# Performance work log

Measured on AMD Instinct MI355X. Metric: run time of the kernel, lower is better.

## Reference

```python
import jax, jax.numpy as jnp
import numpy as np

B, C, H, W = 16, 256, 64, 64
NH = 4                      # num_heads
HD = C // NH                # head_dim = 64
G = 32                      # GroupNorm groups
EPS = 1e-5


def setup_inputs() -> dict:
    key = jax.random.key(0)
    ks = jax.random.split(key, 7)
    x = jax.random.normal(ks[0], (B, C, H, W), dtype=jnp.float32)
    gn_w = jnp.ones((C,), dtype=jnp.float32)
    gn_b = jnp.zeros((C,), dtype=jnp.float32)
    qkv_w = jax.random.normal(ks[1], (3 * C, C), dtype=jnp.float32) * 0.02
    qkv_b = jnp.zeros((3 * C,), dtype=jnp.float32)
    out_w = jax.random.normal(ks[2], (C, C), dtype=jnp.float32) * 0.02
    out_b = jnp.zeros((C,), dtype=jnp.float32)
    return {"x": x, "gn_w": gn_w, "gn_b": gn_b, "qkv_w": qkv_w,
            "qkv_b": qkv_b, "out_w": out_w, "out_b": out_b}


def _group_norm(x, w, b):
    # x: (B, C, H, W); normalize over each of G groups of channels (+ spatial)
    Bx, Cx, Hx, Wx = x.shape
    xr = x.reshape(Bx, G, -1)
    mean = xr.mean(axis=-1, keepdims=True)
    var = xr.var(axis=-1, keepdims=True)
    h = ((xr - mean) * jax.lax.rsqrt(var + EPS)).reshape(Bx, Cx, Hx, Wx)
    return h * w[None, :, None, None] + b[None, :, None, None]


def reference(x, gn_w, gn_b, qkv_w, qkv_b, out_w, out_b):
    Bx, Cx, Hx, Wx = x.shape
    N = Hx * Wx
    h = _group_norm(x, gn_w, gn_b)
    # 1x1 conv == channel matmul
    qkv = jnp.einsum('oc,bchw->bohw', qkv_w, h) + qkv_b[None, :, None, None]
    q, k, v = jnp.split(qkv, 3, axis=1)
    # b (h d) y x -> b h d n
    q = q.reshape(Bx, NH, HD, N)
    k = k.reshape(Bx, NH, HD, N)
    v = v.reshape(Bx, NH, HD, N)
    q = jax.nn.softmax(q, axis=-1)   # over spatial positions n
    k = jax.nn.softmax(k, axis=-2)   # over head_dim d
    # context = k @ v^T : (b,h,d,d)
    context = jnp.einsum('bhdn,bhen->bhde', k, v)
    # out = context^T @ q : (b,h,d,n)
    out = jnp.einsum('bhde,bhdn->bhen', context, q)
    out = out.reshape(Bx, Cx, Hx, Wx)
    out = jnp.einsum('oc,bchw->bohw', out_w, out) + out_b[None, :, None, None]
    return x + out
```

## Files before the change

### kernel.cpp

```cpp
#include <hip/hip_runtime.h>


typedef __bf16 bf16x8 __attribute__((ext_vector_type(8)));
typedef __bf16 bf16x4 __attribute__((ext_vector_type(4)));
typedef __bf16 bf16x2 __attribute__((ext_vector_type(2)));
typedef float  f32x4  __attribute__((ext_vector_type(4)));

__device__ __forceinline__ float wave_red_sum(float v) {
#pragma unroll
    for (int off = 32; off > 0; off >>= 1) v += __shfl_xor(v, off, 64);
    return v;
}
__device__ __forceinline__ float wave_red_max(float v) {
#pragma unroll
    for (int off = 32; off > 0; off >>= 1) v = fmaxf(v, __shfl_xor(v, off, 64));
    return v;
}

__global__ __launch_bounds__(256)
void gn_stats_kernel(const float* __restrict__ x, const float* __restrict__ gw,
                     const float* __restrict__ gb, const float* __restrict__ qw,
                     float2* __restrict__ scsh, __bf16* __restrict__ wb)
{
    const int blk = blockIdx.x;
    const int b = blk >> 5, g = blk & 31;
    const int tid = threadIdx.x;
    const int lane = tid & 63, wid = tid >> 6;
    const size_t xbase = ((size_t)(b * 256 + g * 8)) * 4096;

    {
        const int ci = (blk * 256 + tid) * 2;
        if (ci < 196608) {
            const float2 f = *(const float2*)(qw + ci);
            bf16x2 t; t[0] = (__bf16)f.x; t[1] = (__bf16)f.y;
            *(bf16x2*)(wb + ci) = t;
        }
    }

    float s1 = 0.f, s2 = 0.f;
#pragma unroll
    for (int it = 0; it < 32; it++) {
        const int idx = (it * 256 + tid) * 4;
        const float4 v4 = *(const float4*)(x + xbase + idx);
        s1 += v4.x + v4.y + v4.z + v4.w;
        s2 += v4.x * v4.x + v4.y * v4.y + v4.z * v4.z + v4.w * v4.w;
    }
    __shared__ float red[8];
    float s1w = wave_red_sum(s1);
    float s2w = wave_red_sum(s2);
    if (lane == 0) { red[wid] = s1w; red[4 + wid] = s2w; }
    __syncthreads();
    const float mean = (red[0] + red[1] + red[2] + red[3]) * (1.0f / 32768.0f);
    const float ms   = (red[4] + red[5] + red[6] + red[7]) * (1.0f / 32768.0f);
    const float inv  = rsqrtf(fmaxf(ms - mean * mean, 0.f) + 1e-5f);

    if (tid < 8) {
        const int c = g * 8 + tid;
        const float sc = gw[c] * inv;
        const float sh = gb[c] - mean * sc;
        scsh[b * 256 + c] = make_float2(sc, sh);
    }
}

__global__ __launch_bounds__(256)
void gemm1_kernel(const __bf16* __restrict__ wbf,
                  const float* __restrict__ x,
                  const float* __restrict__ bias,
                  const float2* __restrict__ scsh,
                  __bf16* __restrict__ qkv)
{
    __shared__ __align__(16) __bf16 lds_bt[64 * 264];
    __shared__ __align__(16) char  lds_a[256 * 64];
    __shared__ float2 lscsh[256];

    const int tid  = threadIdx.x;
    const int lane = tid & 63;
    const int wid  = tid >> 6;
    const int quad = lane >> 4;
    const int tcol = lane & 15;
    const int wm   = wid * 64;
    const int n0   = blockIdx.x * 64;
    const int b    = n0 >> 12;
    const int nn   = n0 & 4095;

    lscsh[tid] = scsh[b * 256 + tid];
    __syncthreads();

    const int sn = tid & 63;
    const int cq = tid >> 6;
    const float* xs = x + (size_t)b * 1048576 + nn + sn;
#pragma unroll
    for (int iter = 0; iter < 4; iter++) {
        const int cbase = cq * 64 + iter * 16;
        bf16x8 o0, o1;
#pragma unroll
        for (int j = 0; j < 16; j++) {
            const int c = cbase + j;
            const float2 ss = lscsh[c];
            const float f = xs[(size_t)c * 4096];
            const __bf16 v = (__bf16)(f * ss.x + ss.y);
            if (j < 8) o0[j] = v; else o1[j - 8] = v;
        }
        __bf16* dst = &lds_bt[sn * 264 + cbase];
        *(bf16x8*)dst       = o0;
        *(bf16x8*)(dst + 8) = o1;
    }

    const int r_   = tid >> 1;
    const int ah   = tid & 1;
    const int h16  = ah * 16;
    const int aswz = (r_ >> 1) & 3;
    const int ch0  = (((ah * 2)     + aswz) & 3) * 16;
    const int ch1  = (((ah * 2 + 1) + aswz) & 3) * 16;
    const __bf16* abase = wbf + (size_t)r_ * 256 + h16;

    bf16x8 a0 = *(const bf16x8*)(abase);
    bf16x8 a1 = *(const bf16x8*)(abase + 8);
    bf16x8 a2 = *(const bf16x8*)(abase + 32768);
    bf16x8 a3 = *(const bf16x8*)(abase + 32768 + 8);

    for (int mt = 0; mt < 3; mt++) {
        f32x4 acc[4][4];
#pragma unroll
        for (int i = 0; i < 4; i++)
#pragma unroll
            for (int j = 0; j < 4; j++) acc[i][j] = {0.f, 0.f, 0.f, 0.f};

        for (int kt = 0; kt < 256; kt += 32) {
            __syncthreads();
            *(bf16x8*)&lds_a[r_ * 64         + ch0] = a0;
            *(bf16x8*)&lds_a[r_ * 64         + ch1] = a1;
            *(bf16x8*)&lds_a[(r_ + 128) * 64 + ch0] = a2;
            *(bf16x8*)&lds_a[(r_ + 128) * 64 + ch1] = a3;
            __syncthreads();

            const int last = (kt == 224);
            const int nkt  = last ? 0 : kt + 32;
            const int nmt  = last ? mt + 1 : mt;
            if (nmt < 3) {
                const __bf16* ap = abase + (size_t)nmt * 65536 + nkt;
                a0 = *(const bf16x8*)(ap);
                a1 = *(const bf16x8*)(ap + 8);
                a2 = *(const bf16x8*)(ap + 32768);
                a3 = *(const bf16x8*)(ap + 32768 + 8);
            }

            bf16x8 af[4];
#pragma unroll
            for (int mi = 0; mi < 4; mi++) {
                const int m = wm + mi * 16 + tcol;
                af[mi] = *(const bf16x8*)&lds_a[m * 64
                         + ((quad + ((m >> 1) & 3)) & 3) * 16];
            }
            bf16x8 bfr[4];
#pragma unroll
            for (int ni = 0; ni < 4; ni++)
                bfr[ni] = *(const bf16x8*)&lds_bt[(ni * 16 + tcol) * 264
                                                 + kt + quad * 8];
#pragma unroll
            for (int mi = 0; mi < 4; mi++)
#pragma unroll
                for (int ni = 0; ni < 4; ni++)
                    acc[mi][ni] = __builtin_amdgcn_mfma_f32_16x16x32_bf16(
                        af[mi], bfr[ni], acc[mi][ni], 0, 0, 0);
        }

#pragma unroll
        for (int mi = 0; mi < 4; mi++) {
#pragma unroll
            for (int r = 0; r < 4; r++) {
                const int grow = mt * 256 + wm + mi * 16 + quad * 4 + r;
                const float bv = bias[grow];
#pragma unroll
                for (int ni = 0; ni < 4; ni++) {
                    const int gcol = n0 + ni * 16 + tcol;
                    qkv[(size_t)grow * 65536 + gcol] = (__bf16)(acc[mi][ni][r] + bv);
                }
            }
        }
    }
}

__global__ __launch_bounds__(256)
void qstats_kernel(const __bf16* __restrict__ qkv, float2* __restrict__ qst)
{
    const int o = blockIdx.x >> 4;
    const int b = blockIdx.x & 15;
    const int tid = threadIdx.x;
    const int lane = tid & 63, wid = tid >> 6;
    const size_t base = (size_t)o * 65536 + (size_t)b * 4096;

    float v[16];
    float m = -INFINITY;
#pragma unroll
    for (int s = 0; s < 16; s++) {
        v[s] = (float)qkv[base + s * 256 + tid];
        m = fmaxf(m, v[s]);
    }
    __shared__ float red[4];
    float wmx = wave_red_max(m);
    if (lane == 0) red[wid] = wmx;
    __syncthreads();
    m = fmaxf(fmaxf(red[0], red[1]), fmaxf(red[2], red[3]));
    __syncthreads();
    float sum = 0.f;
#pragma unroll
    for (int s = 0; s < 16; s++) sum += __expf(v[s] - m);
    float wsm = wave_red_sum(sum);
    if (lane == 0) red[wid] = wsm;
    __syncthreads();
    if (tid == 0)
        qst[o * 16 + b] = make_float2(m, 1.0f / (red[0] + red[1] + red[2] + red[3]));
}

__global__ __launch_bounds__(256)
void ctx_mfma_kernel(const __bf16* __restrict__ qkv, float* __restrict__ ctx)
{
    const int bh = blockIdx.x >> 3, kc = blockIdx.x & 7;
    const int b = bh >> 2, hh = bh & 3;
    __shared__ __align__(16) __bf16 lk[64 * 72], lv[64 * 72];
    __shared__ float smax[4][64], ssum[4][64];
    const int tid = threadIdx.x;
    const int lane = tid & 63, wid = tid >> 6;
    const int quad = lane >> 4, tcol = lane & 15;
    const int eh = (wid & 1) * 32, dh = (wid >> 1) * 32;
    const int col = tid & 63, dq = tid >> 6;
    const int sd = tid >> 2, snn = (tid & 3) * 16;

    f32x4 acc[2][2];
#pragma unroll
    for (int i = 0; i < 2; i++)
#pragma unroll
        for (int j = 0; j < 2; j++) acc[i][j] = {0.f, 0.f, 0.f, 0.f};

    const size_t kbase = (size_t)(256 + hh * 64) * 65536 + (size_t)b * 4096 + kc * 512;
    const size_t vbase = (size_t)(512 + hh * 64) * 65536 + (size_t)b * 4096 + kc * 512;

    for (int nc = 0; nc < 512; nc += 64) {
        __syncthreads();
        {
            const __bf16* ks = qkv + kbase + (size_t)sd * 65536 + nc + snn;
            *(bf16x8*)&lk[sd * 72 + snn]     = *(const bf16x8*)ks;
            *(bf16x8*)&lk[sd * 72 + snn + 8] = *(const bf16x8*)(ks + 8);
            const __bf16* vs = qkv + vbase + (size_t)sd * 65536 + nc + snn;
            *(bf16x8*)&lv[sd * 72 + snn]     = *(const bf16x8*)vs;
            *(bf16x8*)&lv[sd * 72 + snn + 8] = *(const bf16x8*)(vs + 8);
        }
        __syncthreads();

        float kvv[16];
        float pm = -INFINITY;
#pragma unroll
        for (int i = 0; i < 16; i++) {
            kvv[i] = (float)lk[(dq * 16 + i) * 72 + col];
            pm = fmaxf(pm, kvv[i]);
        }
        smax[dq][col] = pm;
        __syncthreads();
        const float m = fmaxf(fmaxf(smax[0][col], smax[1][col]),
                              fmaxf(smax[2][col], smax[3][col]));
        float ps = 0.f;
#pragma unroll
        for (int i = 0; i < 16; i++) { kvv[i] = __expf(kvv[i] - m); ps += kvv[i]; }
        ssum[dq][col] = ps;
        __syncthreads();
        const float inv = 1.0f / (ssum[0][col] + ssum[1][col] + ssum[2][col] + ssum[3][col]);
#pragma unroll
        for (int i = 0; i < 16; i++)
            lk[(dq * 16 + i) * 72 + col] = (__bf16)(kvv[i] * inv);
        __syncthreads();

#pragma unroll
        for (int k2 = 0; k2 < 64; k2 += 32) {
            bf16x8 af[2], bfr[2];
#pragma unroll
            for (int mi = 0; mi < 2; mi++)
                af[mi] = *(const bf16x8*)&lv[(eh + mi * 16 + tcol) * 72 + k2 + quad * 8];
#pragma unroll
            for (int ni = 0; ni < 2; ni++)
                bfr[ni] = *(const bf16x8*)&lk[(dh + ni * 16 + tcol) * 72 + k2 + quad * 8];
#pragma unroll
            for (int mi = 0; mi < 2; mi++)
#pragma unroll
                for (int ni = 0; ni < 2; ni++)
                    acc[mi][ni] = __builtin_amdgcn_mfma_f32_16x16x32_bf16(
                        af[mi], bfr[ni], acc[mi][ni], 0, 0, 0);
        }
    }
    float* cb = ctx + (size_t)bh * 4096;
#pragma unroll
    for (int mi = 0; mi < 2; mi++)
#pragma unroll
        for (int ni = 0; ni < 2; ni++)
#pragma unroll
            for (int r = 0; r < 4; r++) {
                const int e = eh + mi * 16 + quad * 4 + r;
                const int d = dh + ni * 16 + tcol;
                atomicAdd(&cb[e * 64 + d], acc[mi][ni][r]);
            }
}

__global__ __launch_bounds__(256)
void w2_kernel(const float* __restrict__ ctx, const float* __restrict__ out_w,
               __bf16* __restrict__ w2)
{
    const int bh = blockIdx.x;
    const int b = bh >> 2, hh = bh & 3;
    const int tid = threadIdx.x;

    __shared__ __align__(16) float lctx[4096];
    const float* csrc = ctx + (size_t)bh * 4096;
#pragma unroll
    for (int i = 0; i < 4; i++)
        ((float4*)lctx)[tid + i * 256] = ((const float4*)csrc)[tid + i * 256];
    __syncthreads();

    float acc[64];
#pragma unroll
    for (int d = 0; d < 64; d++) acc[d] = 0.f;

    const float* wrow = out_w + (size_t)tid * 256 + hh * 64;
    for (int e = 0; e < 64; e++) {
        const float w = wrow[e];
#pragma unroll
        for (int d4 = 0; d4 < 64; d4 += 4) {
            const float4 c4 = *(const float4*)&lctx[e * 64 + d4];
            acc[d4 + 0] += w * c4.x;
            acc[d4 + 1] += w * c4.y;
            acc[d4 + 2] += w * c4.z;
            acc[d4 + 3] += w * c4.w;
        }
    }
    __bf16* dst = w2 + (size_t)b * 65536 + (size_t)tid * 256 + hh * 64;
#pragma unroll
    for (int d4 = 0; d4 < 64; d4 += 4) {
        bf16x4 t;
        t[0] = (__bf16)acc[d4 + 0]; t[1] = (__bf16)acc[d4 + 1];
        t[2] = (__bf16)acc[d4 + 2]; t[3] = (__bf16)acc[d4 + 3];
        *(bf16x4*)(dst + d4) = t;
    }
}

__global__ __launch_bounds__(256)
void gemm2_kernel(const __bf16* __restrict__ w2,
                  const __bf16* __restrict__ qkv,
                  const float2* __restrict__ qst,
                  const float* __restrict__ bias,
                  const float* __restrict__ xres,
                  float* __restrict__ out)
{
    __shared__ __align__(16) __bf16 lds_bt[128 * 264];
    __shared__ __align__(16) __bf16 lds_a[128 * 40];
    __shared__ float2 lqst[256];

    const int tid  = threadIdx.x;
    const int lane = tid & 63;
    const int wid  = tid >> 6;
    const int quad = lane >> 4;
    const int tcol = lane & 15;
    const int wm   = (wid & 1) * 64;
    const int wn   = (wid >> 1) * 64;
    const int n0   = blockIdx.x * 128;
    const int b    = n0 >> 12;

    lqst[tid] = qst[tid * 16 + b];
    __syncthreads();

    const int sn    = tid & 127;
    const int chalf = tid >> 7;
    const int swz   = (sn >> 3) & 3;
#pragma unroll
    for (int iter = 0; iter < 8; iter++) {
        const int cbase = iter * 32 + chalf * 16;
        bf16x8 o0, o1;
        const __bf16* qs = qkv + n0 + sn;
#pragma unroll
        for (int j = 0; j < 16; j++) {
            const int c = cbase + j;
            const float2 qq = lqst[c];
            const float f = (float)qs[(size_t)c * 65536];
            const __bf16 v = (__bf16)(__expf(f - qq.x) * qq.y);
            if (j < 8) o0[j] = v; else o1[j - 8] = v;
        }
        const int chunk = iter * 2 + chalf;
        const int chSw  = chunk ^ swz;
        __bf16* dst = &lds_bt[sn * 264 + chSw * 16];
        *(bf16x8*)dst       = o0;
        *(bf16x8*)(dst + 8) = o1;
    }

    const int arow = tid >> 1, k16 = (tid & 1) * 16;

    for (int mt = 0; mt < 2; mt++) {
        const int m0 = mt * 128;
        f32x4 acc[4][4];
#pragma unroll
        for (int i = 0; i < 4; i++)
#pragma unroll
            for (int j = 0; j < 4; j++) acc[i][j] = {0.f, 0.f, 0.f, 0.f};

        for (int kt = 0; kt < 256; kt += 32) {
            __syncthreads();
            {
                const __bf16* src = w2 + (size_t)b * 65536
                                  + (size_t)(m0 + arow) * 256 + kt + k16;
                const bf16x8 o0 = *(const bf16x8*)(src);
                const bf16x8 o1 = *(const bf16x8*)(src + 8);
                *(bf16x8*)&lds_a[arow * 40 + k16]     = o0;
                *(bf16x8*)&lds_a[arow * 40 + k16 + 8] = o1;
            }
            __syncthreads();

            bf16x8 af[4];
#pragma unroll
            for (int mi = 0; mi < 4; mi++)
                af[mi] = *(const bf16x8*)&lds_a[(wm + mi * 16 + tcol) * 40 + quad * 8];
            bf16x8 bfr[4];
#pragma unroll
            for (int ni = 0; ni < 4; ni++) {
                const int n = wn + ni * 16 + tcol;
                const int k = kt + quad * 8;
                const int chSw = (k >> 4) ^ ((n >> 3) & 3);
                bfr[ni] = *(const bf16x8*)&lds_bt[n * 264 + chSw * 16 + (k & 15)];
            }
#pragma unroll
            for (int mi = 0; mi < 4; mi++)
#pragma unroll
                for (int ni = 0; ni < 4; ni++)
                    acc[mi][ni] = __builtin_amdgcn_mfma_f32_16x16x32_bf16(
                        af[mi], bfr[ni], acc[mi][ni], 0, 0, 0);
        }

#pragma unroll
        for (int mi = 0; mi < 4; mi++) {
#pragma unroll
            for (int r = 0; r < 4; r++) {
                const int grow = m0 + wm + mi * 16 + quad * 4 + r;
                const float bv = bias[grow];
#pragma unroll
                for (int ni = 0; ni < 4; ni++) {
                    const int gcol = n0 + wn + ni * 16 + tcol;
                    const int n = gcol & 4095;
                    const size_t oidx = ((size_t)(b * 256 + grow)) * 4096 + n;
                    out[oidx] = acc[mi][ni][r] + bv + xres[oidx];
                }
            }
        }
    }
}

extern "C" void kernel_launch(void* const* d_in, const int* in_sizes, int n_in,
                              void* d_out, int out_size, void* d_ws, size_t ws_size,
                              hipStream_t stream)
{
    const float* x     = (const float*)d_in[0];
    const float* gn_w  = (const float*)d_in[1];
    const float* gn_b  = (const float*)d_in[2];
    const float* qkv_w = (const float*)d_in[3];
    const float* qkv_b = (const float*)d_in[4];
    const float* out_w = (const float*)d_in[5];
    const float* out_b = (const float*)d_in[6];
    float* out = (float*)d_out;

    char* ws = (char*)d_ws;
    __bf16* qkv  = (__bf16*)ws;
    float*  ctx  = (float*)(ws + (size_t)100663296);
    float2* scsh = (float2*)(ws + (size_t)101711872);
    float2* qst  = (float2*)(ws + (size_t)101744640);
    __bf16* wbf  = (__bf16*)(ws + (size_t)101777408);
    __bf16* w2   = qkv + (size_t)256 * 65536;

    hipMemsetAsync(ctx, 0, 262144 * sizeof(float), stream);
    gn_stats_kernel<<<512, 256, 0, stream>>>(x, gn_w, gn_b, qkv_w, scsh, wbf);
    gemm1_kernel<<<1024, 256, 0, stream>>>(wbf, x, qkv_b, scsh, qkv);
    qstats_kernel<<<4096, 256, 0, stream>>>(qkv, qst);
    ctx_mfma_kernel<<<512, 256, 0, stream>>>(qkv, ctx);
    w2_kernel<<<64, 256, 0, stream>>>(ctx, out_w, w2);
    gemm2_kernel<<<512, 256, 0, stream>>>(w2, qkv, qst, out_b, x, out);
}
```

Measured before the change: 265.5 us.

## Precompute K softmax stats in stats kernel and apply during ctx tile load

Moves the per-position softmax-over-head-dim max and sum for K out of ctx_mfma_kernel into extra blocks of the merged Q/K stats kernel, writing them to the output buffer as scratch. The ctx kernel then normalizes K while loading each tile into LDS, using double-buffered stats in shared memory. This removes three block barriers and the LDS reductions per tile. In exchange, K is read from global memory twice more by strided per-d loads in the stats pass.

```diff
diff --git a/kernel.cpp b/kernel.cpp
--- a/kernel.cpp
+++ b/kernel.cpp
@@ -182,49 +182,68 @@
 }
 
 __global__ __launch_bounds__(256)
-void qstats_kernel(const __bf16* __restrict__ qkv, float2* __restrict__ qst)
-{
-    const int o = blockIdx.x >> 4;
-    const int b = blockIdx.x & 15;
+void stats_kernel(const __bf16* __restrict__ qkv, float2* __restrict__ qst,
+                  float2* __restrict__ kst)
+{
     const int tid = threadIdx.x;
-    const int lane = tid & 63, wid = tid >> 6;
-    const size_t base = (size_t)o * 65536 + (size_t)b * 4096;
-
-    float v[16];
-    float m = -INFINITY;
-#pragma unroll
-    for (int s = 0; s < 16; s++) {
-        v[s] = (float)qkv[base + s * 256 + tid];
-        m = fmaxf(m, v[s]);
-    }
-    __shared__ float red[4];
-    float wmx = wave_red_max(m);
-    if (lane == 0) red[wid] = wmx;
-    __syncthreads();
-    m = fmaxf(fmaxf(red[0], red[1]), fmaxf(red[2], red[3]));
-    __syncthreads();
-    float sum = 0.f;
-#pragma unroll
-    for (int s = 0; s < 16; s++) sum += __expf(v[s] - m);
-    float wsm = wave_red_sum(sum);
-    if (lane == 0) red[wid] = wsm;
-    __syncthreads();
-    if (tid == 0)
-        qst[o * 16 + b] = make_float2(m, 1.0f / (red[0] + red[1] + red[2] + red[3]));
-}
-
-__global__ __launch_bounds__(256)
-void ctx_mfma_kernel(const __bf16* __restrict__ qkv, float* __restrict__ ctx)
+    if (blockIdx.x < 4096) {
+        const int o = blockIdx.x >> 4;
+        const int b = blockIdx.x & 15;
+        const int lane = tid & 63, wid = tid >> 6;
+        const size_t base = (size_t)o * 65536 + (size_t)b * 4096;
+
+        float v[16];
+        float m = -INFINITY;
+#pragma unroll
+        for (int s = 0; s < 16; s++) {
+            v[s] = (float)qkv[base + s * 256 + tid];
+            m = fmaxf(m, v[s]);
+        }
+        __shared__ float red[4];
+        float wmx = wave_red_max(m);
+        if (lane == 0) red[wid] = wmx;
+        __syncthreads();
+        m = fmaxf(fmaxf(red[0], red[1]), fmaxf(red[2], red[3]));
+        __syncthreads();
+        float sum = 0.f;
+#pragma unroll
+        for (int s = 0; s < 16; s++) sum += __expf(v[s] - m);
+        float wsm = wave_red_sum(sum);
+        if (lane == 0) red[wid] = wsm;
+        __syncthreads();
+        if (tid == 0)
+            qst[o * 16 + b] = make_float2(m, 1.0f / (red[0] + red[1] + red[2] + red[3]));
+    } else {
+        const int idx = blockIdx.x - 4096;
+        const int bh = idx >> 4, chunk = idx & 15;
+        const int b = bh >> 2, hh = bh & 3;
+        const int n = chunk * 256 + tid;
+        const __bf16* kp = qkv + (size_t)(256 + hh * 64) * 65536
+                         + (size_t)b * 4096 + n;
+
+        float m = -INFINITY;
+        for (int d = 0; d < 64; d++)
+            m = fmaxf(m, (float)kp[(size_t)d * 65536]);
+        float s = 0.f;
+        for (int d = 0; d < 64; d++)
+            s += __expf((float)kp[(size_t)d * 65536] - m);
+        kst[(size_t)bh * 4096 + n] = make_float2(m, 1.0f / s);
+    }
+}
+
+__global__ __launch_bounds__(256)
+void ctx_mfma_kernel(const __bf16* __restrict__ qkv,
+                     const float2* __restrict__ kst,
+                     float* __restrict__ ctx)
 {
     const int bh = blockIdx.x >> 3, kc = blockIdx.x & 7;
     const int b = bh >> 2, hh = bh & 3;
     __shared__ __align__(16) __bf16 lk[64 * 72], lv[64 * 72];
-    __shared__ float smax[4][64], ssum[4][64];
+    __shared__ float2 lsmv[2][64];
     const int tid = threadIdx.x;
     const int lane = tid & 63, wid = tid >> 6;
     const int quad = lane >> 4, tcol = lane & 15;
     const int eh = (wid & 1) * 32, dh = (wid >> 1) * 32;
-    const int col = tid & 63, dq = tid >> 6;
     const int sd = tid >> 2, snn = (tid & 3) * 16;
 
     f32x4 acc[2][2];
@@ -235,39 +254,33 @@
 
     const size_t kbase = (size_t)(256 + hh * 64) * 65536 + (size_t)b * 4096 + kc * 512;
     const size_t vbase = (size_t)(512 + hh * 64) * 65536 + (size_t)b * 4096 + kc * 512;
+    const float2* kstp = kst + (size_t)bh * 4096 + kc * 512;
+
+    if (tid < 64) lsmv[0][tid] = kstp[tid];
 
     for (int nc = 0; nc < 512; nc += 64) {
+        const int p = (nc >> 6) & 1;
         __syncthreads();
         {
             const __bf16* ks = qkv + kbase + (size_t)sd * 65536 + nc + snn;
-            *(bf16x8*)&lk[sd * 72 + snn]     = *(const bf16x8*)ks;
-            *(bf16x8*)&lk[sd * 72 + snn + 8] = *(const bf16x8*)(ks + 8);
+            const bf16x8 k0 = *(const bf16x8*)ks;
+            const bf16x8 k1 = *(const bf16x8*)(ks + 8);
+            bf16x8 o0, o1;
+#pragma unroll
+            for (int j = 0; j < 8; j++) {
+                const float2 s0 = lsmv[p][snn + j];
+                const float2 s1 = lsmv[p][snn + 8 + j];
+                o0[j] = (__bf16)(__expf((float)k0[j] - s0.x) * s0.y);
+                o1[j] = (__bf16)(__expf((float)k1[j] - s1.x) * s1.y);
+            }
+            *(bf16x8*)&lk[sd * 72 + snn]     = o0;
+            *(bf16x8*)&lk[sd * 72 + snn + 8] = o1;
             const __bf16* vs = qkv + vbase + (size_t)sd * 65536 + nc + snn;
             *(bf16x8*)&lv[sd * 72 + snn]     = *(const bf16x8*)vs;
             *(bf16x8*)&lv[sd * 72 + snn + 8] = *(const bf16x8*)(vs + 8);
         }
-        __syncthreads();
-
-        float kvv[16];
-        float pm = -INFINITY;
-#pragma unroll
-        for (int i = 0; i < 16; i++) {
-            kvv[i] = (float)lk[(dq * 16 + i) * 72 + col];
-            pm = fmaxf(pm, kvv[i]);
-        }
-        smax[dq][col] = pm;
-        __syncthreads();
-        const float m = fmaxf(fmaxf(smax[0][col], smax[1][col]),
-                              fmaxf(smax[2][col], smax[3][col]));
-        float ps = 0.f;
-#pragma unroll
-        for (int i = 0; i < 16; i++) { kvv[i] = __expf(kvv[i] - m); ps += kvv[i]; }
-        ssum[dq][col] = ps;
-        __syncthreads();
-        const float inv = 1.0f / (ssum[0][col] + ssum[1][col] + ssum[2][col] + ssum[3][col]);
-#pragma unroll
-        for (int i = 0; i < 16; i++)
-            lk[(dq * 16 + i) * 72 + col] = (__bf16)(kvv[i] * inv);
+        if (tid < 64 && nc + 64 < 512)
+            lsmv[p ^ 1][tid] = kstp[nc + 64 + tid];
         __syncthreads();
 
 #pragma unroll
@@ -469,12 +482,13 @@
     float2* qst  = (float2*)(ws + (size_t)101744640);
     __bf16* wbf  = (__bf16*)(ws + (size_t)101777408);
     __bf16* w2   = qkv + (size_t)256 * 65536;
+    float2* kst  = (float2*)d_out;
 
     hipMemsetAsync(ctx, 0, 262144 * sizeof(float), stream);
     gn_stats_kernel<<<512, 256, 0, stream>>>(x, gn_w, gn_b, qkv_w, scsh, wbf);
     gemm1_kernel<<<1024, 256, 0, stream>>>(wbf, x, qkv_b, scsh, qkv);
-    qstats_kernel<<<4096, 256, 0, stream>>>(qkv, qst);
-    ctx_mfma_kernel<<<512, 256, 0, stream>>>(qkv, ctx);
+    stats_kernel<<<5120, 256, 0, stream>>>(qkv, qst, kst);
+    ctx_mfma_kernel<<<512, 256, 0, stream>>>(qkv, kst, ctx);
     w2_kernel<<<64, 256, 0, stream>>>(ctx, out_w, w2);
     gemm2_kernel<<<512, 256, 0, stream>>>(w2, qkv, qst, out_b, x, out);
 }
```

Result: slower. 277.5 us (+4.5%).
